# Optimization experiments

Hardware: AMD Instinct MI355X
Metric: run time of the kernel (lower is better)

Reference implementation:

```python
import jax, jax.numpy as jnp
import numpy as np

B, S, I, H, HI = 1024, 64, 2048, 2048, 2048  # batch, num_high_states, input_dim, hidden_dim, high_dim
L = 4          # num recurrent layers
NH = 16        # num heads
HD = H // NH   # head dim
MAX_STEPS = 100


def setup_inputs() -> dict:
    key = jax.random.key(0)
    ks = iter(jax.random.split(key, 40))
    std = 0.02
    d = {}
    d["x"] = jax.random.normal(next(ks), (B, I), jnp.float32)
    d["high_state"] = jax.random.normal(next(ks), (B, HI), jnp.float32)
    d["high_states_history"] = jax.random.normal(next(ks), (B, S, HI), jnp.float32)
    d["hidden"] = jax.random.normal(next(ks), (L, B, H), jnp.float32) * 0.1
    # input projection + timestep embedding
    d["W_in"] = jax.random.normal(next(ks), (I, H), jnp.float32) * std
    d["b_in"] = jnp.zeros((H,), jnp.float32)
    d["ts_emb"] = jax.random.normal(next(ks), (MAX_STEPS, H), jnp.float32) * std
    # hierarchical attention projections
    d["Wq"] = jax.random.normal(next(ks), (H, H), jnp.float32) * std
    d["bq"] = jnp.zeros((H,), jnp.float32)
    d["Wk"] = jax.random.normal(next(ks), (HI, H), jnp.float32) * std
    d["bk"] = jnp.zeros((H,), jnp.float32)
    d["Wv"] = jax.random.normal(next(ks), (HI, H), jnp.float32) * std
    d["bv"] = jnp.zeros((H,), jnp.float32)
    d["Wo"] = jax.random.normal(next(ks), (H, H), jnp.float32) * std
    d["bo"] = jnp.zeros((H,), jnp.float32)
    # per-layer GRU-like gates, stacked over layers; Linear in = I+H = 2H
    for nm in ("Wu", "Wr", "Ws", "Wc"):
        d[nm] = jax.random.normal(next(ks), (L, 2 * H, H), jnp.float32) * std
    for nm in ("bu", "br", "bs", "bc"):
        d[nm] = jnp.zeros((L, H), jnp.float32)
    # layer norm
    d["ln_g"] = jnp.ones((H,), jnp.float32)
    d["ln_b"] = jnp.zeros((H,), jnp.float32)
    d["timestep"] = 5
    return d


def _forward(x, high_states_history, hidden, W_in, b_in, ts_emb,
             Wq, bq, Wk, bk, Wv, bv, Wo, bo,
             Wu, bu, Wr, br, Ws, bs, Wc, bc, ln_g, ln_b, timestep):
    # input projection + timestep encoding
    x = x @ W_in + b_in + ts_emb[timestep]  # [B,H]
    # hierarchical attention (single query per batch element)
    q = (x @ Wq + bq).reshape(B, NH, HD)
    k = (high_states_history @ Wk + bk).reshape(B, S, NH, HD)
    v = (high_states_history @ Wv + bv).reshape(B, S, NH, HD)
    scores = jnp.einsum("bhd,bshd->bhs", q, k) / np.sqrt(HD).astype(np.float32)
    attn = jax.nn.softmax(scores, axis=-1)  # [B,NH,S]
    ctx = jnp.einsum("bhs,bshd->bhd", attn, v).reshape(B, H)
    x = x + (ctx @ Wo + bo)
    # stacked GRU-like recurrent layers (loop over fixed small L)
    new_hidden = []
    for i in range(L):
        h = hidden[i]
        comb = jnp.concatenate([x, h], axis=1)  # [B,2H]
        u = jax.nn.sigmoid(comb @ Wu[i] + bu[i])
        r = jax.nn.sigmoid(comb @ Wr[i] + br[i])
        s = jax.nn.sigmoid(comb @ Ws[i] + bs[i])
        comb_r = jnp.concatenate([x, r * h], axis=1)
        cand = jax.nn.gelu(comb_r @ Wc[i] + bc[i], approximate=False)
        new_h = (1 - u) * h + u * (s * cand + (1 - s) * h)
        new_hidden.append(new_h)
        x = new_h  # dropout is identity in eval
    # layer norm (eps matches torch default 1e-5)
    mu = jnp.mean(x, axis=-1, keepdims=True)
    var = jnp.mean(jnp.square(x - mu), axis=-1, keepdims=True)
    out = (x - mu) * jax.lax.rsqrt(var + 1e-5) * ln_g + ln_b
    return out, jnp.stack(new_hidden)


def reference(x, high_state, high_states_history, hidden, W_in, b_in, ts_emb,
              Wq, bq, Wk, bk, Wv, bv, Wo, bo,
              Wu, bu, Wr, br, Ws, bs, Wc, bc, ln_g, ln_b, timestep):
    # high_state is accepted by the original signature but unused in the body
    return _forward(x, high_states_history, hidden, W_in, b_in, ts_emb,
                    Wq, bq, Wk, bk, Wv, bv, Wo, bo,
                    Wu, bu, Wr, br, Ws, bs, Wc, bc, ln_g, ln_b, timestep)
```

## Files before the change

### kernel.cpp

```cpp
#include <hip/hip_runtime.h>
#include <hip/hip_bf16.h>
#include <math.h>

#define B_  1024
#define S_  64
#define H_  2048
#define L_  4
#define NH_ 16
#define HD_ 128
#define WSLAB_ ((size_t)2048 * 4096)

typedef __attribute__((ext_vector_type(4))) float floatx4;
typedef __attribute__((ext_vector_type(8))) short shortx8;

__device__ __forceinline__ unsigned short f2bf(float f) {
  union { float f; unsigned int u; } v; v.f = f;
  unsigned int u = v.u;
  return (unsigned short)((u + 0x7fffu + ((u >> 16) & 1u)) >> 16);
}

__device__ __forceinline__ void gload16(const void* g, void* l) {
  __builtin_amdgcn_global_load_lds(
      (const __attribute__((address_space(1))) void*)g,
      (__attribute__((address_space(3))) void*)l, 16, 0, 0);
}

__global__ __launch_bounds__(256) void cvt_bf(
    const float* __restrict__ in, unsigned short* __restrict__ out, int n8)
{
  int i = blockIdx.x * 256 + threadIdx.x;
  if (i >= n8) return;
  const float4* p = (const float4*)in;
  float4 a = p[i * 2], b = p[i * 2 + 1];
  unsigned short o[8] = { f2bf(a.x), f2bf(a.y), f2bf(a.z), f2bf(a.w),
                          f2bf(b.x), f2bf(b.y), f2bf(b.z), f2bf(b.w) };
  ((uint4*)out)[i] = *(uint4*)o;
}

__global__ __launch_bounds__(256) void tconv4(
    const float* __restrict__ s0, const float* __restrict__ s1,
    const float* __restrict__ s2, const float* __restrict__ s3,
    unsigned short* __restrict__ dst, int K)
{
  const float* src = (blockIdx.z == 0) ? s0 : (blockIdx.z == 1) ? s1
                   : (blockIdx.z == 2) ? s2 : s3;
  unsigned short* out = dst + (size_t)blockIdx.z * 2048 * K;
  __shared__ float tile[64][65];
  int k0 = blockIdx.x * 64, n0 = blockIdx.y * 64;
  int t = threadIdx.x;
  int tr = t >> 4, tc = (t & 15) * 4;
  #pragma unroll
  for (int rep = 0; rep < 4; ++rep) {
    int kk = tr + rep * 16;
    float4 v = *(const float4*)(src + (size_t)(k0 + kk) * 2048 + n0 + tc);
    tile[kk][tc] = v.x; tile[kk][tc + 1] = v.y;
    tile[kk][tc + 2] = v.z; tile[kk][tc + 3] = v.w;
  }
  __syncthreads();
  int nr = t >> 2, kc = (t & 3) * 16;
  unsigned short o[16];
  #pragma unroll
  for (int j = 0; j < 16; ++j) o[j] = f2bf(tile[kc + j][nr]);
  *(uint4*)(out + (size_t)(n0 + nr) * K + k0 + kc)     = *(uint4*)&o[0];
  *(uint4*)(out + (size_t)(n0 + nr) * K + k0 + kc + 8) = *(uint4*)&o[8];
}

enum { EPI_XIN = 0, EPI_QB = 1, EPI_X2 = 2, EPI_GRU = 3 };

template<int EPI>
__global__ __launch_bounds__(256) void gemm64(
    int K, int bpitch, int koff,
    const unsigned short* __restrict__ A0,
    const unsigned short* __restrict__ BT,
    const float* __restrict__ b0,
    const float* __restrict__ tse, const int* __restrict__ tsp,
    const float* __restrict__ res,
    const float* __restrict__ Cc, const float* __restrict__ U,
    const float* __restrict__ Sg, const float* __restrict__ Hf,
    float* __restrict__ Cf, unsigned short* __restrict__ Cb)
{
  const int t = threadIdx.x, wid = t >> 6, lane = t & 63, lr = lane & 15, lg = lane >> 4;
  const int wr = wid >> 1, wc = wid & 1;
  const int g = blockIdx.x;
  const int m_base = (g >> 5) * 64;
  const int n_base = (g & 31) * 64;
  __shared__ unsigned short lds_a[64 * 32];
  __shared__ unsigned short lds_b[64 * 32];
  floatx4 acc[2][2] = {};
  const int row = t >> 2, kc = t & 3;
  const int kcs = kc ^ ((row >> 1) & 3);
  const int nkt = K >> 5;
  for (int kt = 0; kt < nkt; ++kt) {
    int gk = kt * 32 + kcs * 8;
    gload16(A0 + (size_t)(m_base + row) * K + gk, &lds_a[wid * 512]);
    gload16(BT + (size_t)(n_base + row) * bpitch + koff + gk, &lds_b[wid * 512]);
    __syncthreads();
    const int sl = lg ^ ((lr >> 1) & 3);
    shortx8 af[2], bfv[2];
    #pragma unroll
    for (int mt = 0; mt < 2; ++mt)
      af[mt] = *(shortx8*)&lds_a[(wr * 32 + mt * 16 + lr) * 32 + sl * 8];
    #pragma unroll
    for (int nt = 0; nt < 2; ++nt)
      bfv[nt] = *(shortx8*)&lds_b[(wc * 32 + nt * 16 + lr) * 32 + sl * 8];
    #pragma unroll
    for (int mt = 0; mt < 2; ++mt)
      #pragma unroll
      for (int nt = 0; nt < 2; ++nt)
        acc[mt][nt] = __builtin_amdgcn_mfma_f32_16x16x32_bf16(af[mt], bfv[nt], acc[mt][nt], 0, 0, 0);
    __syncthreads();
  }
  int ts = 0;
  if (EPI == EPI_XIN) ts = tsp[0];
  #pragma unroll
  for (int mt = 0; mt < 2; ++mt)
  #pragma unroll
  for (int nt = 0; nt < 2; ++nt)
  #pragma unroll
  for (int j = 0; j < 4; ++j) {
    int r = m_base + wr * 32 + mt * 16 + lg * 4 + j;
    int col = n_base + wc * 32 + nt * 16 + lr;
    size_t idx = (size_t)r * 2048 + col;
    float v = acc[mt][nt][j] + b0[col];
    if (EPI == EPI_XIN) {
      v += tse[(size_t)ts * 2048 + col];
      Cf[idx] = v; Cb[idx] = f2bf(v);
    } else if (EPI == EPI_QB) {
      Cb[idx] = f2bf(v);
    } else if (EPI == EPI_X2) {
      v += res[idx]; Cb[idx] = f2bf(v);
    } else {
      v += Cc[idx];
      float gl = 0.5f * v * (1.f + erff(v * 0.70710678118654752f));
      float u = U[idx], s = Sg[idx], hh = Hf[idx];
      float nh = (1.f - u) * hh + u * (s * gl + (1.f - s) * hh);
      Cf[idx] = nh; Cb[idx] = f2bf(nh);
    }
  }
}

__global__ __launch_bounds__(256) void gemm_gates(
    const unsigned short* __restrict__ Ax, const unsigned short* __restrict__ Ah,
    const unsigned short* __restrict__ TW,
    const float* __restrict__ bu, const float* __restrict__ br, const float* __restrict__ bs,
    const float* __restrict__ Hf,
    float* __restrict__ U, float* __restrict__ Sg,
    unsigned short* __restrict__ rh, float* __restrict__ Cc)
{
  const int t = threadIdx.x, wid = t >> 6, lane = t & 63, lr = lane & 15, lg = lane >> 4;
  const int wr = wid >> 1, wc = wid & 1;
  const int g = blockIdx.x;
  const int m_base = (g >> 6) * 128;
  const int pan = g & 63;
  const int n_base = (pan & 15) * 128;
  const int z = pan >> 4;
  const unsigned short* BTz = TW + (size_t)z * WSLAB_;
  __shared__ unsigned short lds_a[128 * 32];
  __shared__ unsigned short lds_b[128 * 32];
  floatx4 acc[4][4] = {};
  const int nkt = (z == 3) ? 64 : 128;
  for (int kt = 0; kt < nkt; ++kt) {
    #pragma unroll
    for (int is = 0; is < 2; ++is) {
      int idx = is * 256 + t;
      int row = idx >> 2, kc = idx & 3;
      int kcs = kc ^ ((row >> 1) & 3);
      int gk = kt * 32 + kcs * 8;
      const unsigned short* ga;
      if (z == 3 || gk < 2048) ga = Ax + (size_t)(m_base + row) * 2048 + gk;
      else                     ga = Ah + (size_t)(m_base + row) * 2048 + (gk - 2048);
      gload16(ga, &lds_a[(is * 256 + wid * 64) * 8]);
    }
    #pragma unroll
    for (int is = 0; is < 2; ++is) {
      int idx = is * 256 + t;
      int row = idx >> 2, kc = idx & 3;
      int kcs = kc ^ ((row >> 1) & 3);
      int gk = kt * 32 + kcs * 8;
      gload16(BTz + (size_t)(n_base + row) * 4096 + gk, &lds_b[(is * 256 + wid * 64) * 8]);
    }
    __syncthreads();
    const int sl = lg ^ ((lr >> 1) & 3);
    shortx8 af[4], bfv[4];
    #pragma unroll
    for (int mt = 0; mt < 4; ++mt)
      af[mt] = *(shortx8*)&lds_a[(wr * 64 + mt * 16 + lr) * 32 + sl * 8];
    #pragma unroll
    for (int nt = 0; nt < 4; ++nt)
      bfv[nt] = *(shortx8*)&lds_b[(wc * 64 + nt * 16 + lr) * 32 + sl * 8];
    #pragma unroll
    for (int mt = 0; mt < 4; ++mt)
      #pragma unroll
      for (int nt = 0; nt < 4; ++nt)
        acc[mt][nt] = __builtin_amdgcn_mfma_f32_16x16x32_bf16(af[mt], bfv[nt], acc[mt][nt], 0, 0, 0);
    __syncthreads();
  }
  #pragma unroll
  for (int mt = 0; mt < 4; ++mt)
  #pragma unroll
  for (int nt = 0; nt < 4; ++nt)
  #pragma unroll
  for (int j = 0; j < 4; ++j) {
    int row = m_base + wr * 64 + mt * 16 + lg * 4 + j;
    int col = n_base + wc * 64 + nt * 16 + lr;
    size_t idx = (size_t)row * 2048 + col;
    float v = acc[mt][nt][j];
    if (z == 0)      U[idx]  = 1.f / (1.f + expf(-(v + bu[col])));
    else if (z == 1) rh[idx] = f2bf((1.f / (1.f + expf(-(v + br[col])))) * Hf[idx]);
    else if (z == 2) Sg[idx] = 1.f / (1.f + expf(-(v + bs[col])));
    else             Cc[idx] = v;
  }
}

__global__ __launch_bounds__(256) void gemm_t(
    const unsigned short* __restrict__ Q, const unsigned short* __restrict__ Wk,
    unsigned short* __restrict__ T)
{
  const int t = threadIdx.x, wid = t >> 6, lane = t & 63, lr = lane & 15, lg = lane >> 4;
  const int wr = wid >> 1, wc = wid & 1;
  const int h = blockIdx.z, m_base = blockIdx.x * 64, n_base = blockIdx.y * 128;
  __shared__ unsigned short lds_a[64 * 32], lds_b[128 * 32];
  floatx4 acc[2][4] = {};
  const int arow = t >> 2, akc = t & 3;
  const int akcs = akc ^ ((arow >> 1) & 3);
  for (int kt = 0; kt < 4; ++kt) {
    gload16(Q + (size_t)(m_base + arow) * 2048 + h * 128 + kt * 32 + akcs * 8,
            &lds_a[wid * 512]);
    #pragma unroll
    for (int is = 0; is < 2; ++is) {
      int idx = is * 256 + t;
      int row = idx >> 2, kc = idx & 3;
      int kcs = kc ^ ((row >> 1) & 3);
      gload16(Wk + (size_t)(n_base + row) * 2048 + h * 128 + kt * 32 + kcs * 8,
              &lds_b[(is * 256 + wid * 64) * 8]);
    }
    __syncthreads();
    const int sl = lg ^ ((lr >> 1) & 3);
    shortx8 af[2], bfv[4];
    #pragma unroll
    for (int mt = 0; mt < 2; ++mt)
      af[mt] = *(shortx8*)&lds_a[(wr * 32 + mt * 16 + lr) * 32 + sl * 8];
    #pragma unroll
    for (int nt = 0; nt < 4; ++nt)
      bfv[nt] = *(shortx8*)&lds_b[(wc * 64 + nt * 16 + lr) * 32 + sl * 8];
    #pragma unroll
    for (int mt = 0; mt < 2; ++mt)
      #pragma unroll
      for (int nt = 0; nt < 4; ++nt)
        acc[mt][nt] = __builtin_amdgcn_mfma_f32_16x16x32_bf16(af[mt], bfv[nt], acc[mt][nt], 0, 0, 0);
    __syncthreads();
  }
  #pragma unroll
  for (int mt = 0; mt < 2; ++mt)
  #pragma unroll
  for (int nt = 0; nt < 4; ++nt)
  #pragma unroll
  for (int j = 0; j < 4; ++j) {
    int row_o = m_base + wr * 32 + mt * 16 + lg * 4 + j;
    int col   = n_base + wc * 64 + nt * 16 + lr;
    T[((size_t)row_o * 16 + h) * 2048 + col] = f2bf(acc[mt][nt][j]);
  }
}

__global__ __launch_bounds__(256) void attn_fused(
    const unsigned short* __restrict__ T, const float* __restrict__ hist,
    unsigned short* __restrict__ Wb)
{
  const int t = threadIdx.x;
  const int wid = t >> 6, lane = t & 63, lr = lane & 15, lg = lane >> 4;
  const int b = blockIdx.x;
  __shared__ unsigned short lds_t[16 * 72];
  __shared__ unsigned short lds_h[64 * 72];
  __shared__ float sc[16 * 68];
  __shared__ float ps[64 * 16];
  floatx4 acc = {};
  for (int kt = 0; kt < 32; ++kt) {
    { int row = t >> 4, c4 = t & 15;
      int k = kt * 64 + c4 * 4;
      ushort4 v = *(const ushort4*)(T + ((size_t)b * 16 + row) * 2048 + k);
      *(ushort4*)&lds_t[row * 72 + c4 * 4] = v; }
    #pragma unroll
    for (int rep = 0; rep < 4; ++rep) {
      int idx = t + rep * 256;
      int srow = idx >> 4, c4 = idx & 15;
      int k = kt * 64 + c4 * 4;
      float4 hv = *(const float4*)(hist + ((size_t)b * 64 + srow) * 2048 + k);
      ushort4 uv; uv.x = f2bf(hv.x); uv.y = f2bf(hv.y); uv.z = f2bf(hv.z); uv.w = f2bf(hv.w);
      *(ushort4*)&lds_h[srow * 72 + c4 * 4] = uv;
    }
    __syncthreads();
    #pragma unroll
    for (int ks = 0; ks < 2; ++ks) {
      shortx8 af = *(shortx8*)&lds_t[lr * 72 + ks * 32 + lg * 8];
      shortx8 bv = *(shortx8*)&lds_h[(wid * 16 + lr) * 72 + ks * 32 + lg * 8];
      acc = __builtin_amdgcn_mfma_f32_16x16x32_bf16(af, bv, acc, 0, 0, 0);
    }
    __syncthreads();
  }
  #pragma unroll
  for (int j = 0; j < 4; ++j)
    sc[(lg * 4 + j) * 68 + wid * 16 + lr] = acc[j] * 0.088388347648318447f;
  __syncthreads();
  if (t < 64) {
    int h = t >> 2, qd = t & 3;
    float vv[16];
    float m = -1e30f;
    #pragma unroll
    for (int zz = 0; zz < 16; ++zz) { vv[zz] = sc[h * 68 + qd * 16 + zz]; m = fmaxf(m, vv[zz]); }
    m = fmaxf(m, __shfl_xor(m, 1)); m = fmaxf(m, __shfl_xor(m, 2));
    float sum = 0.f;
    #pragma unroll
    for (int zz = 0; zz < 16; ++zz) { vv[zz] = expf(vv[zz] - m); sum += vv[zz]; }
    sum += __shfl_xor(sum, 1); sum += __shfl_xor(sum, 2);
    float inv = 1.f / sum;
    #pragma unroll
    for (int zz = 0; zz < 16; ++zz)
      ps[(qd * 16 + zz) * 16 + h] = vv[zz] * inv;
  }
  __syncthreads();
  const int i0 = t * 8;
  floatx4 wacc[16][2] = {};
  const floatx4* ps4 = (const floatx4*)ps;
  for (int s = 0; s < 64; ++s) {
    const float* hp = hist + ((size_t)b * 64 + s) * 2048 + i0;
    float4 h4a = *(const float4*)hp;
    float4 h4b = *(const float4*)(hp + 4);
    floatx4 hva = { h4a.x, h4a.y, h4a.z, h4a.w };
    floatx4 hvb = { h4b.x, h4b.y, h4b.z, h4b.w };
    #pragma unroll
    for (int hq = 0; hq < 4; ++hq) {
      floatx4 p = ps4[s * 4 + hq];
      wacc[hq * 4 + 0][0] += p.x * hva; wacc[hq * 4 + 0][1] += p.x * hvb;
      wacc[hq * 4 + 1][0] += p.y * hva; wacc[hq * 4 + 1][1] += p.y * hvb;
      wacc[hq * 4 + 2][0] += p.z * hva; wacc[hq * 4 + 2][1] += p.z * hvb;
      wacc[hq * 4 + 3][0] += p.w * hva; wacc[hq * 4 + 3][1] += p.w * hvb;
    }
  }
  #pragma unroll
  for (int h = 0; h < 16; ++h) {
    unsigned short o[8];
    #pragma unroll
    for (int j = 0; j < 4; ++j) { o[j] = f2bf(wacc[h][0][j]); o[4 + j] = f2bf(wacc[h][1][j]); }
    *(uint4*)(Wb + ((size_t)b * 16 + h) * 2048 + i0) = *(uint4*)o;
  }
}

__global__ __launch_bounds__(256) void gemm_ctx(
    const unsigned short* __restrict__ Wb, const unsigned short* __restrict__ WvT,
    const float* __restrict__ bv, unsigned short* __restrict__ ctx)
{
  const int t = threadIdx.x, wid = t >> 6, lane = t & 63, lr = lane & 15, lg = lane >> 4;
  const int wr = wid >> 1, wc = wid & 1;
  const int h = blockIdx.z, m_base = blockIdx.x * 64;
  __shared__ unsigned short lds_a[64 * 32], lds_b[128 * 32];
  floatx4 acc[2][4] = {};
  const int row = t >> 2, kc = t & 3;
  const int kcs = kc ^ ((row >> 1) & 3);
  for (int kt = 0; kt < 64; ++kt) {
    int gk = kt * 32 + kcs * 8;
    gload16(Wb  + ((size_t)(m_base + row) * 16 + h) * 2048 + gk, &lds_a[wid * 512]);
    gload16(WvT + (size_t)(h * 128 + row) * 2048 + gk,           &lds_b[wid * 512]);
    gload16(WvT + (size_t)(h * 128 + 64 + row) * 2048 + gk,      &lds_b[2048 + wid * 512]);
    __syncthreads();
    const int sl = lg ^ ((lr >> 1) & 3);
    shortx8 af[2], bfv[4];
    #pragma unroll
    for (int mt = 0; mt < 2; ++mt)
      af[mt] = *(shortx8*)&lds_a[(wr * 32 + mt * 16 + lr) * 32 + sl * 8];
    #pragma unroll
    for (int nt = 0; nt < 4; ++nt)
      bfv[nt] = *(shortx8*)&lds_b[(wc * 64 + nt * 16 + lr) * 32 + sl * 8];
    #pragma unroll
    for (int mt = 0; mt < 2; ++mt)
      #pragma unroll
      for (int nt = 0; nt < 4; ++nt)
        acc[mt][nt] = __builtin_amdgcn_mfma_f32_16x16x32_bf16(af[mt], bfv[nt], acc[mt][nt], 0, 0, 0);
    __syncthreads();
  }
  #pragma unroll
  for (int mt = 0; mt < 2; ++mt)
  #pragma unroll
  for (int nt = 0; nt < 4; ++nt)
  #pragma unroll
  for (int j = 0; j < 4; ++j) {
    int row_o = m_base + wr * 32 + mt * 16 + lg * 4 + j;
    int cl = wc * 64 + nt * 16 + lr;
    int gcol = h * 128 + cl;
    ctx[(size_t)row_o * 2048 + gcol] = f2bf(acc[mt][nt][j] + bv[gcol]);
  }
}

__global__ __launch_bounds__(256) void lnorm(
    const float* __restrict__ X, const float* __restrict__ gma,
    const float* __restrict__ bta, float* __restrict__ out)
{
  const int row = blockIdx.x, t = threadIdx.x;
  float4 a = *(const float4*)(X + (size_t)row * 2048 + t * 4);
  float4 c = *(const float4*)(X + (size_t)row * 2048 + 1024 + t * 4);
  float sum = a.x + a.y + a.z + a.w + c.x + c.y + c.z + c.w;
  float sq = a.x*a.x + a.y*a.y + a.z*a.z + a.w*a.w + c.x*c.x + c.y*c.y + c.z*c.z + c.w*c.w;
  #pragma unroll
  for (int off = 1; off < 64; off <<= 1) {
    sum += __shfl_xor(sum, off);
    sq  += __shfl_xor(sq, off);
  }
  __shared__ float red[8];
  int wid = t >> 6, lane = t & 63;
  if (lane == 0) { red[wid] = sum; red[wid + 4] = sq; }
  __syncthreads();
  sum = red[0] + red[1] + red[2] + red[3];
  sq  = red[4] + red[5] + red[6] + red[7];
  float mu = sum * (1.f / 2048.f);
  float var = sq * (1.f / 2048.f) - mu * mu;
  float rs = rsqrtf(var + 1e-5f);
  const float* pa = &a.x; const float* pc = &c.x;
  #pragma unroll
  for (int j = 0; j < 4; ++j) {
    int col = t * 4 + j;
    out[(size_t)row * 2048 + col] = (pa[j] - mu) * rs * gma[col] + bta[col];
  }
  #pragma unroll
  for (int j = 0; j < 4; ++j) {
    int col = 1024 + t * 4 + j;
    out[(size_t)row * 2048 + col] = (pc[j] - mu) * rs * gma[col] + bta[col];
  }
}

extern "C" void kernel_launch(void* const* d_in, const int* in_sizes, int n_in,
                              void* d_out, int out_size, void* d_ws, size_t ws_size,
                              hipStream_t stream) {
  (void)in_sizes; (void)n_in; (void)out_size; (void)ws_size;
  const float* x      = (const float*)d_in[0];
  const float* hist   = (const float*)d_in[2];
  const float* hidden = (const float*)d_in[3];
  const float* W_in   = (const float*)d_in[4];
  const float* b_in   = (const float*)d_in[5];
  const float* ts_emb = (const float*)d_in[6];
  const float* Wq     = (const float*)d_in[7];
  const float* bq     = (const float*)d_in[8];
  const float* Wk     = (const float*)d_in[9];
  const float* Wv     = (const float*)d_in[11];
  const float* bv     = (const float*)d_in[12];
  const float* Wo     = (const float*)d_in[13];
  const float* bo     = (const float*)d_in[14];
  const float* Wu     = (const float*)d_in[15];
  const float* Wr     = (const float*)d_in[16];
  const float* Wsg    = (const float*)d_in[17];
  const float* Wc     = (const float*)d_in[18];
  const float* bu     = (const float*)d_in[19];
  const float* br     = (const float*)d_in[20];
  const float* bs     = (const float*)d_in[21];
  const float* bc     = (const float*)d_in[22];
  const float* ln_g   = (const float*)d_in[23];
  const float* ln_b   = (const float*)d_in[24];
  const int*   tsp    = (const int*)d_in[25];
  float* out = (float*)d_out;

  const size_t BH = (size_t)B_ * H_;
  char* w = (char*)d_ws;
  auto take = [&](size_t bytes) { char* p = w; w += bytes; return p; };

  unsigned short* TW   = (unsigned short*)take((size_t)4 * WSLAB_ * 2);
  unsigned short* Tb   = (unsigned short*)take((size_t)B_ * 16 * 2048 * 2);
  unsigned short* WT4  = (unsigned short*)take((size_t)4 * H_ * H_ * 2);
  unsigned short* WinT = WT4;
  unsigned short* WqT  = WT4 + (size_t)H_ * H_;
  unsigned short* WvT  = WT4 + (size_t)2 * H_ * H_;
  unsigned short* WoT  = WT4 + (size_t)3 * H_ * H_;
  unsigned short* Wkb  = (unsigned short*)take((size_t)H_ * H_ * 2);
  unsigned short* x_bf   = (unsigned short*)take(BH * 2);
  unsigned short* h_bf   = (unsigned short*)take((size_t)L_ * BH * 2);
  unsigned short* xin_bf = (unsigned short*)take(BH * 2);
  unsigned short* q_bf   = (unsigned short*)take(BH * 2);
  unsigned short* ctx_bf = (unsigned short*)take(BH * 2);
  unsigned short* x2_bf  = (unsigned short*)take(BH * 2);
  unsigned short* rh_bf  = (unsigned short*)take(BH * 2);
  unsigned short* xa     = (unsigned short*)take(BH * 2);
  unsigned short* xb     = (unsigned short*)take(BH * 2);
  float* U   = (float*)take(BH * 4);
  float* Sg  = (float*)take(BH * 4);
  float* Cc  = (float*)take(BH * 4);
  float* XIN = out;

  dim3 blk(256);

  cvt_bf<<<dim3(1024), blk, 0, stream>>>(x, x_bf, (int)(BH / 8));
  cvt_bf<<<dim3(4096), blk, 0, stream>>>(hidden, h_bf, (int)(L_ * BH / 8));
  cvt_bf<<<dim3(2048), blk, 0, stream>>>(Wk, Wkb, (int)((size_t)H_ * H_ / 8));
  tconv4<<<dim3(32, 32, 4), blk, 0, stream>>>(W_in, Wq, Wv, Wo, WT4, 2048);

  gemm64<EPI_XIN><<<dim3(512), blk, 0, stream>>>(
      2048, 2048, 0, x_bf, WinT, b_in, ts_emb, tsp, nullptr,
      nullptr, nullptr, nullptr, nullptr, XIN, xin_bf);
  gemm64<EPI_QB><<<dim3(512), blk, 0, stream>>>(
      2048, 2048, 0, xin_bf, WqT, bq, nullptr, nullptr, nullptr,
      nullptr, nullptr, nullptr, nullptr, nullptr, q_bf);
  gemm_t<<<dim3(16, 16, 16), blk, 0, stream>>>(q_bf, Wkb, Tb);
  attn_fused<<<dim3(1024), blk, 0, stream>>>(Tb, hist, Tb);
  gemm_ctx<<<dim3(16, 1, 16), blk, 0, stream>>>(Tb, WvT, bv, ctx_bf);
  gemm64<EPI_X2><<<dim3(512), blk, 0, stream>>>(
      2048, 2048, 0, ctx_bf, WoT, bo, nullptr, nullptr, XIN,
      nullptr, nullptr, nullptr, nullptr, nullptr, x2_bf);

  unsigned short* xcur = x2_bf;
  for (int i = 0; i < L_; ++i) {
    const float* h_i = hidden + (size_t)i * BH;
    float* nh_f = out + BH + (size_t)i * BH;
    unsigned short* nh_b = (i & 1) ? xb : xa;
    tconv4<<<dim3(64, 32, 4), blk, 0, stream>>>(
        Wu + (size_t)i * WSLAB_, Wr + (size_t)i * WSLAB_,
        Wsg + (size_t)i * WSLAB_, Wc + (size_t)i * WSLAB_, TW, 4096);
    gemm_gates<<<dim3(512), blk, 0, stream>>>(
        xcur, h_bf + (size_t)i * BH, TW,
        bu + (size_t)i * H_, br + (size_t)i * H_, bs + (size_t)i * H_,
        h_i, U, Sg, rh_bf, Cc);
    gemm64<EPI_GRU><<<dim3(512), blk, 0, stream>>>(
        2048, 4096, 2048, rh_bf, TW + (size_t)3 * WSLAB_,
        bc + (size_t)i * H_, nullptr, nullptr, nullptr,
        Cc, U, Sg, h_i, nh_f, nh_b);
    xcur = nh_b;
  }

  lnorm<<<dim3(1024), blk, 0, stream>>>(out + BH + (size_t)3 * BH, ln_g, ln_b, out);
}
```

Before: 1.337 ms.

## Overlap next-layer weight transpose with gate GEMM and widen GEMM tiles

Double-buffers the transposed GRU weight slabs. The bf16 transpose of layer i+1 now runs as extra blocks inside the layer-i gate GEMM launch, so conversion overlaps compute and the separate per-layer tconv launches go away. The gate GEMM tile shrinks to 64 rows, doubling its block count. The 64x64 gemm64 becomes a 512-thread 64x128 gemm_w that also absorbs the old gemm_ctx via a CTX epilogue. It costs an extra 64 MB weight buffer and mixes heterogeneous blocks in one grid, which can hurt scheduling balance.

```diff
diff --git a/kernel.cpp b/kernel.cpp
--- a/kernel.cpp
+++ b/kernel.cpp
@@ -65,10 +65,10 @@
   *(uint4*)(out + (size_t)(n0 + nr) * K + k0 + kc + 8) = *(uint4*)&o[8];
 }
 
-enum { EPI_XIN = 0, EPI_QB = 1, EPI_X2 = 2, EPI_GRU = 3 };
+enum { EPI_XIN = 0, EPI_QB = 1, EPI_X2 = 2, EPI_GRU = 3, EPI_CTX = 4 };
 
 template<int EPI>
-__global__ __launch_bounds__(256) void gemm64(
+__global__ __launch_bounds__(512) void gemm_w(
     int K, int bpitch, int koff,
     const unsigned short* __restrict__ A0,
     const unsigned short* __restrict__ BT,
@@ -80,20 +80,33 @@
     float* __restrict__ Cf, unsigned short* __restrict__ Cb)
 {
   const int t = threadIdx.x, wid = t >> 6, lane = t & 63, lr = lane & 15, lg = lane >> 4;
-  const int wr = wid >> 1, wc = wid & 1;
+  const int wr = wid >> 2, wc = wid & 3;
   const int g = blockIdx.x;
-  const int m_base = (g >> 5) * 64;
-  const int n_base = (g & 31) * 64;
+  const int m_base = (g >> 4) * 64;
+  const int pn = g & 15;
   __shared__ unsigned short lds_a[64 * 32];
-  __shared__ unsigned short lds_b[64 * 32];
+  __shared__ unsigned short lds_b[128 * 32];
   floatx4 acc[2][2] = {};
-  const int row = t >> 2, kc = t & 3;
-  const int kcs = kc ^ ((row >> 1) & 3);
+  const int arow = t >> 2, akc = t & 3;
+  const int akcs = akc ^ ((arow >> 1) & 3);
+  const int brow = t >> 2, bkc = t & 3;
+  const int bkcs = bkc ^ ((brow >> 1) & 3);
   const int nkt = K >> 5;
   for (int kt = 0; kt < nkt; ++kt) {
-    int gk = kt * 32 + kcs * 8;
-    gload16(A0 + (size_t)(m_base + row) * K + gk, &lds_a[wid * 512]);
-    gload16(BT + (size_t)(n_base + row) * bpitch + koff + gk, &lds_b[wid * 512]);
+    if (t < 256) {
+      int gk = kt * 32 + akcs * 8;
+      const unsigned short* ga;
+      if (EPI == EPI_CTX) ga = A0 + ((size_t)(m_base + arow) * 16 + pn) * 2048 + gk;
+      else                ga = A0 + (size_t)(m_base + arow) * K + gk;
+      gload16(ga, &lds_a[wid * 512]);
+    }
+    {
+      int gk = kt * 32 + bkcs * 8;
+      const unsigned short* gb;
+      if (EPI == EPI_CTX) gb = BT + (size_t)(pn * 128 + brow) * 2048 + gk;
+      else                gb = BT + (size_t)((pn & 15) * 128 + brow) * bpitch + koff + gk;
+      gload16(gb, &lds_b[wid * 512]);
+    }
     __syncthreads();
     const int sl = lg ^ ((lr >> 1) & 3);
     shortx8 af[2], bfv[2];
@@ -118,9 +131,9 @@
   for (int nt = 0; nt < 2; ++nt)
   #pragma unroll
   for (int j = 0; j < 4; ++j) {
-    int r = m_base + wr * 32 + mt * 16 + lg * 4 + j;
-    int col = n_base + wc * 32 + nt * 16 + lr;
-    size_t idx = (size_t)r * 2048 + col;
+    int row = m_base + wr * 32 + mt * 16 + lg * 4 + j;
+    int col = pn * 128 + wc * 32 + nt * 16 + lr;
+    size_t idx = (size_t)row * 2048 + col;
     float v = acc[mt][nt][j] + b0[col];
     if (EPI == EPI_XIN) {
       v += tse[(size_t)ts * 2048 + col];
@@ -129,6 +142,8 @@
       Cb[idx] = f2bf(v);
     } else if (EPI == EPI_X2) {
       v += res[idx]; Cb[idx] = f2bf(v);
+    } else if (EPI == EPI_CTX) {
+      Cb[idx] = f2bf(v);
     } else {
       v += Cc[idx];
       float gl = 0.5f * v * (1.f + erff(v * 0.70710678118654752f));
@@ -139,76 +154,106 @@
   }
 }
 
-__global__ __launch_bounds__(256) void gemm_gates(
+__global__ __launch_bounds__(256, 4) void gates_tconv(
     const unsigned short* __restrict__ Ax, const unsigned short* __restrict__ Ah,
     const unsigned short* __restrict__ TW,
     const float* __restrict__ bu, const float* __restrict__ br, const float* __restrict__ bs,
     const float* __restrict__ Hf,
     float* __restrict__ U, float* __restrict__ Sg,
-    unsigned short* __restrict__ rh, float* __restrict__ Cc)
-{
-  const int t = threadIdx.x, wid = t >> 6, lane = t & 63, lr = lane & 15, lg = lane >> 4;
-  const int wr = wid >> 1, wc = wid & 1;
-  const int g = blockIdx.x;
-  const int m_base = (g >> 6) * 128;
-  const int pan = g & 63;
-  const int n_base = (pan & 15) * 128;
-  const int z = pan >> 4;
-  const unsigned short* BTz = TW + (size_t)z * WSLAB_;
-  __shared__ unsigned short lds_a[128 * 32];
-  __shared__ unsigned short lds_b[128 * 32];
-  floatx4 acc[4][4] = {};
-  const int nkt = (z == 3) ? 64 : 128;
-  for (int kt = 0; kt < nkt; ++kt) {
-    #pragma unroll
-    for (int is = 0; is < 2; ++is) {
-      int idx = is * 256 + t;
-      int row = idx >> 2, kc = idx & 3;
-      int kcs = kc ^ ((row >> 1) & 3);
-      int gk = kt * 32 + kcs * 8;
-      const unsigned short* ga;
-      if (z == 3 || gk < 2048) ga = Ax + (size_t)(m_base + row) * 2048 + gk;
-      else                     ga = Ah + (size_t)(m_base + row) * 2048 + (gk - 2048);
-      gload16(ga, &lds_a[(is * 256 + wid * 64) * 8]);
-    }
-    #pragma unroll
-    for (int is = 0; is < 2; ++is) {
-      int idx = is * 256 + t;
-      int row = idx >> 2, kc = idx & 3;
-      int kcs = kc ^ ((row >> 1) & 3);
-      int gk = kt * 32 + kcs * 8;
-      gload16(BTz + (size_t)(n_base + row) * 4096 + gk, &lds_b[(is * 256 + wid * 64) * 8]);
-    }
-    __syncthreads();
-    const int sl = lg ^ ((lr >> 1) & 3);
-    shortx8 af[4], bfv[4];
-    #pragma unroll
-    for (int mt = 0; mt < 4; ++mt)
-      af[mt] = *(shortx8*)&lds_a[(wr * 64 + mt * 16 + lr) * 32 + sl * 8];
-    #pragma unroll
-    for (int nt = 0; nt < 4; ++nt)
-      bfv[nt] = *(shortx8*)&lds_b[(wc * 64 + nt * 16 + lr) * 32 + sl * 8];
-    #pragma unroll
-    for (int mt = 0; mt < 4; ++mt)
+    unsigned short* __restrict__ rh, float* __restrict__ Cc,
+    const float* __restrict__ Wun, const float* __restrict__ Wrn,
+    const float* __restrict__ Wsn, const float* __restrict__ Wcn,
+    unsigned short* __restrict__ TWnext)
+{
+  __shared__ __align__(16) float smem[4224];
+  const int t = threadIdx.x;
+  if (blockIdx.x < 1024) {
+    unsigned short* lds_a = (unsigned short*)smem;
+    unsigned short* lds_b = (unsigned short*)smem + 2048;
+    const int wid = t >> 6, lane = t & 63, lr = lane & 15, lg = lane >> 4;
+    const int wr = wid >> 1, wc = wid & 1;
+    const int g = blockIdx.x;
+    const int m_base = (g >> 6) * 64;
+    const int pan = g & 63;
+    const int n_base = (pan & 15) * 128;
+    const int z = pan >> 4;
+    const unsigned short* BTz = TW + (size_t)z * WSLAB_;
+    floatx4 acc[2][4] = {};
+    const int nkt = (z == 3) ? 64 : 128;
+    const int arow = t >> 2, akc = t & 3;
+    const int akcs = akc ^ ((arow >> 1) & 3);
+    for (int kt = 0; kt < nkt; ++kt) {
+      {
+        int gk = kt * 32 + akcs * 8;
+        const unsigned short* ga;
+        if (z == 3 || gk < 2048) ga = Ax + (size_t)(m_base + arow) * 2048 + gk;
+        else                     ga = Ah + (size_t)(m_base + arow) * 2048 + (gk - 2048);
+        gload16(ga, &lds_a[wid * 512]);
+      }
+      #pragma unroll
+      for (int is = 0; is < 2; ++is) {
+        int idx = is * 256 + t;
+        int row = idx >> 2, kc = idx & 3;
+        int kcs = kc ^ ((row >> 1) & 3);
+        int gk = kt * 32 + kcs * 8;
+        gload16(BTz + (size_t)(n_base + row) * 4096 + gk, &lds_b[(is * 256 + wid * 64) * 8]);
+      }
+      __syncthreads();
+      const int sl = lg ^ ((lr >> 1) & 3);
+      shortx8 af[2], bfv[4];
+      #pragma unroll
+      for (int mt = 0; mt < 2; ++mt)
+        af[mt] = *(shortx8*)&lds_a[(wr * 32 + mt * 16 + lr) * 32 + sl * 8];
       #pragma unroll
       for (int nt = 0; nt < 4; ++nt)
-        acc[mt][nt] = __builtin_amdgcn_mfma_f32_16x16x32_bf16(af[mt], bfv[nt], acc[mt][nt], 0, 0, 0);
-    __syncthreads();
-  }
-  #pragma unroll
-  for (int mt = 0; mt < 4; ++mt)
-  #pragma unroll
-  for (int nt = 0; nt < 4; ++nt)
-  #pragma unroll
-  for (int j = 0; j < 4; ++j) {
-    int row = m_base + wr * 64 + mt * 16 + lg * 4 + j;
-    int col = n_base + wc * 64 + nt * 16 + lr;
-    size_t idx = (size_t)row * 2048 + col;
-    float v = acc[mt][nt][j];
-    if (z == 0)      U[idx]  = 1.f / (1.f + expf(-(v + bu[col])));
-    else if (z == 1) rh[idx] = f2bf((1.f / (1.f + expf(-(v + br[col])))) * Hf[idx]);
-    else if (z == 2) Sg[idx] = 1.f / (1.f + expf(-(v + bs[col])));
-    else             Cc[idx] = v;
+        bfv[nt] = *(shortx8*)&lds_b[(wc * 64 + nt * 16 + lr) * 32 + sl * 8];
+      #pragma unroll
+      for (int mt = 0; mt < 2; ++mt)
+        #pragma unroll
+        for (int nt = 0; nt < 4; ++nt)
+          acc[mt][nt] = __builtin_amdgcn_mfma_f32_16x16x32_bf16(af[mt], bfv[nt], acc[mt][nt], 0, 0, 0);
+      __syncthreads();
+    }
+    #pragma unroll
+    for (int mt = 0; mt < 2; ++mt)
+    #pragma unroll
+    for (int nt = 0; nt < 4; ++nt)
+    #pragma unroll
+    for (int j = 0; j < 4; ++j) {
+      int row = m_base + wr * 32 + mt * 16 + lg * 4 + j;
+      int col = n_base + wc * 64 + nt * 16 + lr;
+      size_t idx = (size_t)row * 2048 + col;
+      float v = acc[mt][nt][j];
+      if (z == 0)      U[idx]  = 1.f / (1.f + expf(-(v + bu[col])));
+      else if (z == 1) rh[idx] = f2bf((1.f / (1.f + expf(-(v + br[col])))) * Hf[idx]);
+      else if (z == 2) Sg[idx] = 1.f / (1.f + expf(-(v + bs[col])));
+      else             Cc[idx] = v;
+    }
+  } else {
+    if (TWnext == nullptr) return;
+    float (*tile)[65] = (float(*)[65])smem;
+    int bid = blockIdx.x - 1024;
+    int z = bid >> 11;
+    int rem = bid & 2047;
+    int k0 = (rem >> 5) * 64;
+    int n0 = (rem & 31) * 64;
+    const float* src = (z == 0) ? Wun : (z == 1) ? Wrn : (z == 2) ? Wsn : Wcn;
+    unsigned short* outp = TWnext + (size_t)z * WSLAB_;
+    int tr = t >> 4, tc = (t & 15) * 4;
+    #pragma unroll
+    for (int rep = 0; rep < 4; ++rep) {
+      int kk = tr + rep * 16;
+      float4 v = *(const float4*)(src + (size_t)(k0 + kk) * 2048 + n0 + tc);
+      tile[kk][tc] = v.x; tile[kk][tc + 1] = v.y;
+      tile[kk][tc + 2] = v.z; tile[kk][tc + 3] = v.w;
+    }
+    __syncthreads();
+    int nr = t >> 2, kc = (t & 3) * 16;
+    unsigned short o[16];
+    #pragma unroll
+    for (int j = 0; j < 16; ++j) o[j] = f2bf(tile[kc + j][nr]);
+    *(uint4*)(outp + (size_t)(n0 + nr) * 4096 + k0 + kc)     = *(uint4*)&o[0];
+    *(uint4*)(outp + (size_t)(n0 + nr) * 4096 + k0 + kc + 8) = *(uint4*)&o[8];
   }
 }
 
@@ -342,51 +387,6 @@
     #pragma unroll
     for (int j = 0; j < 4; ++j) { o[j] = f2bf(wacc[h][0][j]); o[4 + j] = f2bf(wacc[h][1][j]); }
     *(uint4*)(Wb + ((size_t)b * 16 + h) * 2048 + i0) = *(uint4*)o;
-  }
-}
-
-__global__ __launch_bounds__(256) void gemm_ctx(
-    const unsigned short* __restrict__ Wb, const unsigned short* __restrict__ WvT,
-    const float* __restrict__ bv, unsigned short* __restrict__ ctx)
-{
-  const int t = threadIdx.x, wid = t >> 6, lane = t & 63, lr = lane & 15, lg = lane >> 4;
-  const int wr = wid >> 1, wc = wid & 1;
-  const int h = blockIdx.z, m_base = blockIdx.x * 64;
-  __shared__ unsigned short lds_a[64 * 32], lds_b[128 * 32];
-  floatx4 acc[2][4] = {};
-  const int row = t >> 2, kc = t & 3;
-  const int kcs = kc ^ ((row >> 1) & 3);
-  for (int kt = 0; kt < 64; ++kt) {
-    int gk = kt * 32 + kcs * 8;
-    gload16(Wb  + ((size_t)(m_base + row) * 16 + h) * 2048 + gk, &lds_a[wid * 512]);
-    gload16(WvT + (size_t)(h * 128 + row) * 2048 + gk,           &lds_b[wid * 512]);
-    gload16(WvT + (size_t)(h * 128 + 64 + row) * 2048 + gk,      &lds_b[2048 + wid * 512]);
-    __syncthreads();
-    const int sl = lg ^ ((lr >> 1) & 3);
-    shortx8 af[2], bfv[4];
-    #pragma unroll
-    for (int mt = 0; mt < 2; ++mt)
-      af[mt] = *(shortx8*)&lds_a[(wr * 32 + mt * 16 + lr) * 32 + sl * 8];
-    #pragma unroll
-    for (int nt = 0; nt < 4; ++nt)
-      bfv[nt] = *(shortx8*)&lds_b[(wc * 64 + nt * 16 + lr) * 32 + sl * 8];
-    #pragma unroll
-    for (int mt = 0; mt < 2; ++mt)
-      #pragma unroll
-      for (int nt = 0; nt < 4; ++nt)
-        acc[mt][nt] = __builtin_amdgcn_mfma_f32_16x16x32_bf16(af[mt], bfv[nt], acc[mt][nt], 0, 0, 0);
-    __syncthreads();
-  }
-  #pragma unroll
-  for (int mt = 0; mt < 2; ++mt)
-  #pragma unroll
-  for (int nt = 0; nt < 4; ++nt)
-  #pragma unroll
-  for (int j = 0; j < 4; ++j) {
-    int row_o = m_base + wr * 32 + mt * 16 + lg * 4 + j;
-    int cl = wc * 64 + nt * 16 + lr;
-    int gcol = h * 128 + cl;
-    ctx[(size_t)row_o * 2048 + gcol] = f2bf(acc[mt][nt][j] + bv[gcol]);
   }
 }
 
@@ -460,7 +460,8 @@
   char* w = (char*)d_ws;
   auto take = [&](size_t bytes) { char* p = w; w += bytes; return p; };
 
-  unsigned short* TW   = (unsigned short*)take((size_t)4 * WSLAB_ * 2);
+  unsigned short* TW0  = (unsigned short*)take((size_t)4 * WSLAB_ * 2);
+  unsigned short* TW1  = (unsigned short*)take((size_t)4 * WSLAB_ * 2);
   unsigned short* Tb   = (unsigned short*)take((size_t)B_ * 16 * 2048 * 2);
   unsigned short* WT4  = (unsigned short*)take((size_t)4 * H_ * H_ * 2);
   unsigned short* WinT = WT4;
@@ -483,22 +484,26 @@
   float* XIN = out;
 
   dim3 blk(256);
+  dim3 blkw(512);
 
   cvt_bf<<<dim3(1024), blk, 0, stream>>>(x, x_bf, (int)(BH / 8));
   cvt_bf<<<dim3(4096), blk, 0, stream>>>(hidden, h_bf, (int)(L_ * BH / 8));
   cvt_bf<<<dim3(2048), blk, 0, stream>>>(Wk, Wkb, (int)((size_t)H_ * H_ / 8));
   tconv4<<<dim3(32, 32, 4), blk, 0, stream>>>(W_in, Wq, Wv, Wo, WT4, 2048);
-
-  gemm64<EPI_XIN><<<dim3(512), blk, 0, stream>>>(
+  tconv4<<<dim3(64, 32, 4), blk, 0, stream>>>(Wu, Wr, Wsg, Wc, TW0, 4096);
+
+  gemm_w<EPI_XIN><<<dim3(256), blkw, 0, stream>>>(
       2048, 2048, 0, x_bf, WinT, b_in, ts_emb, tsp, nullptr,
       nullptr, nullptr, nullptr, nullptr, XIN, xin_bf);
-  gemm64<EPI_QB><<<dim3(512), blk, 0, stream>>>(
+  gemm_w<EPI_QB><<<dim3(256), blkw, 0, stream>>>(
       2048, 2048, 0, xin_bf, WqT, bq, nullptr, nullptr, nullptr,
       nullptr, nullptr, nullptr, nullptr, nullptr, q_bf);
   gemm_t<<<dim3(16, 16, 16), blk, 0, stream>>>(q_bf, Wkb, Tb);
   attn_fused<<<dim3(1024), blk, 0, stream>>>(Tb, hist, Tb);
-  gemm_ctx<<<dim3(16, 1, 16), blk, 0, stream>>>(Tb, WvT, bv, ctx_bf);
-  gemm64<EPI_X2><<<dim3(512), blk, 0, stream>>>(
+  gemm_w<EPI_CTX><<<dim3(256), blkw, 0, stream>>>(
+      2048, 2048, 0, Tb, WvT, bv, nullptr, nullptr, nullptr,
+      nullptr, nullptr, nullptr, nullptr, nullptr, ctx_bf);
+  gemm_w<EPI_X2><<<dim3(256), blkw, 0, stream>>>(
       2048, 2048, 0, ctx_bf, WoT, bo, nullptr, nullptr, XIN,
       nullptr, nullptr, nullptr, nullptr, nullptr, x2_bf);
 
@@ -507,15 +512,17 @@
     const float* h_i = hidden + (size_t)i * BH;
     float* nh_f = out + BH + (size_t)i * BH;
     unsigned short* nh_b = (i & 1) ? xb : xa;
-    tconv4<<<dim3(64, 32, 4), blk, 0, stream>>>(
-        Wu + (size_t)i * WSLAB_, Wr + (size_t)i * WSLAB_,
-        Wsg + (size_t)i * WSLAB_, Wc + (size_t)i * WSLAB_, TW, 4096);
-    gemm_gates<<<dim3(512), blk, 0, stream>>>(
-        xcur, h_bf + (size_t)i * BH, TW,
+    unsigned short* TWcur = (i & 1) ? TW1 : TW0;
+    unsigned short* TWnxt = (i < 3) ? ((i & 1) ? TW0 : TW1) : nullptr;
+    int grid = (i < 3) ? 9216 : 1024;
+    size_t off = (size_t)(i + 1) * WSLAB_;
+    gates_tconv<<<dim3(grid), blk, 0, stream>>>(
+        xcur, h_bf + (size_t)i * BH, TWcur,
         bu + (size_t)i * H_, br + (size_t)i * H_, bs + (size_t)i * H_,
-        h_i, U, Sg, rh_bf, Cc);
-    gemm64<EPI_GRU><<<dim3(512), blk, 0, stream>>>(
-        2048, 4096, 2048, rh_bf, TW + (size_t)3 * WSLAB_,
+        h_i, U, Sg, rh_bf, Cc,
+        Wu + off, Wr + off, Wsg + off, Wc + off, TWnxt);
+    gemm_w<EPI_GRU><<<dim3(256), blkw, 0, stream>>>(
+        2048, 4096, 2048, rh_bf, TWcur + (size_t)3 * WSLAB_,
         bc + (size_t)i * H_, nullptr, nullptr, nullptr,
         Cc, U, Sg, h_i, nh_f, nh_b);
     xcur = nh_b;
```

Measured after the change: 1.273 ms. 4.8% less time.
